# Optimization experiments

Hardware: AMD Instinct MI355X
Metric: run time of the kernel (lower is better)

The kernel has to match this reference:

```python
import jax, jax.numpy as jnp
import numpy as np

T, B, N, L = 1024, 2, 10000, 30   # frames, batch(=2, hardcoded in original), vocab, glosses/sample
S = 2 * L + 1                      # blank-interleaved (CTC-extended) label length


def setup_inputs() -> dict:
    key = jax.random.key(0)
    k1, k2 = jax.random.split(key)
    logits = jax.random.normal(k1, (T, B, N), dtype=jnp.float32)
    label = jax.random.randint(k2, (B * L,), 1, N, dtype=jnp.int32)  # real glosses are >=1 (0 is blank)
    logits_len = jnp.full((B,), T, dtype=jnp.int32)
    label_len = jnp.full((B,), L, dtype=jnp.int32)
    return {"logits": logits, "logits_len": logits_len, "label": label, "label_len": label_len}


def _extend(lab):
    # [l1, l2, ...] -> [0, l1, 0, l2, ..., 0]  (blank-interleaved), shape (S,)
    return jnp.zeros((S,), lab.dtype).at[1::2].set(lab)


def _reach_fwd(ext):
    # map_forward[j, i] > 0  <=>  state j reachable from start at time i (CTC forward lattice).
    pad2 = jnp.full((2,), -1, ext.dtype)
    allow2 = (ext != 0) & (ext != jnp.concatenate([pad2, ext[:-2]]))  # skip-2 allowed
    init = jnp.zeros((S,), bool).at[0].set(True).at[1].set(True)

    def step(c, _):
        s1 = jnp.concatenate([jnp.zeros((1,), bool), c[:-1]])
        s2 = jnp.concatenate([jnp.zeros((2,), bool), c[:-2]]) & allow2
        n = c | s1 | s2
        return n, n

    _, outs = jax.lax.scan(step, init, None, length=T - 1)
    return jnp.concatenate([init[None], outs], axis=0)  # (T, S)


def _reach_bwd(ext):
    # map_backward[j, i] > 0  <=>  end reachable from state j at time i.
    pad2 = jnp.full((2,), -1, ext.dtype)
    allow2 = (ext != 0) & (ext != jnp.concatenate([ext[2:], pad2]))
    init = jnp.zeros((S,), bool).at[S - 1].set(True).at[S - 2].set(True)

    def step(c, _):
        s1 = jnp.concatenate([c[1:], jnp.zeros((1,), bool)])
        s2 = jnp.concatenate([c[2:], jnp.zeros((2,), bool)]) & allow2
        n = c | s1 | s2
        return n, n

    _, outs = jax.lax.scan(step, init, None, length=T - 1)
    return jnp.concatenate([outs[::-1], init[None]], axis=0)  # (T, S), time 0..T-1


def _forward(logits, label):
    labels = label.reshape(B, L)
    ext = jax.vmap(_extend)(labels)            # (B, S)
    rf = jax.vmap(_reach_fwd)(ext)             # (B, T, S)
    rb = jax.vmap(_reach_bwd)(ext)             # (B, T, S)
    sel = (rf & rb).astype(logits.dtype)       # map_final != 0 on the lattice

    def per_sample(logit, e, s):
        # mask[t, v] = any lattice state j with ext[j] == v active at time t
        mask = jnp.zeros((T, N), logit.dtype).at[:, e].max(s) > 0
        # original builds final_label as a detached numpy copy of logit at masked entries
        target = jax.lax.stop_gradient(jnp.where(mask, logit, jnp.zeros((), logit.dtype)))
        return jnp.sum((logit - target) ** 2)  # nn.MSELoss(reduction='sum')

    losses = jax.vmap(per_sample)(jnp.transpose(logits, (1, 0, 2)), ext, sel)
    return jnp.mean(losses)  # (loss1 + loss2) / 2


def reference(logits, logits_len, label, label_len):
    # logits_len / label_len are fixed to full lengths (T, L) so shapes stay static.
    return _forward(logits, label)
```

## Files before the change

### kernel.cpp

```cpp
#include <hip/hip_runtime.h>
#include <stdint.h>

typedef unsigned long long u64;

static constexpr int T = 1024;
static constexpr int B = 2;
static constexpr int N = 10000;
static constexpr int L = 30;
static constexpr int S = 2 * L + 1;

static constexpr int CORR_BLK = 256;
static constexpr int SUM_BLK  = 2048;
static constexpr int NBLK     = CORR_BLK + SUM_BLK;

static constexpr u64 ALL   = (1ULL << S) - 1;
static constexpr u64 EVENM = 0x5555555555555555ULL & ((1ULL << S) - 1);

__device__ __forceinline__ float block_reduce(float s) {
    for (int off = 32; off; off >>= 1) s += __shfl_down(s, off, 64);
    __shared__ float tmp[8];
    int lane = threadIdx.x & 63, w = threadIdx.x >> 6;
    int nw = blockDim.x >> 6;
    if (lane == 0) tmp[w] = s;
    __syncthreads();
    float t = 0.f;
    if (threadIdx.x == 0)
        for (int i = 0; i < nw; ++i) t += tmp[i];
    return t;
}

__global__ void k_fused(const float4* __restrict__ x4, const float* __restrict__ x,
                        const int* __restrict__ label, float* __restrict__ out) {
    float s = 0.f;
    if (blockIdx.x < CORR_BLK) {
        __shared__ int labs[B][L];
        __shared__ u64 dups[B][L];
        __shared__ u64 AfS[B], AbS[B];
        int tid = threadIdx.x;
        if (tid < B) {
            int b = tid;
            int lb[L];
            u64 Af = 0, Ab = 0;
            #pragma unroll
            for (int k = 0; k < L; ++k) { lb[k] = label[b * L + k]; labs[b][k] = lb[k]; }
            #pragma unroll
            for (int k = 0; k < L; ++k) {
                u64 bit = 1ULL << (2 * k + 1);
                if (k == 0     || lb[k] != lb[k - 1]) Af |= bit;
                if (k == L - 1 || lb[k] != lb[k + 1]) Ab |= bit;
                u64 d = 0;
                for (int k2 = 0; k2 < k; ++k2)
                    if (lb[k2] == lb[k]) d |= 1ULL << (2 * k2 + 1);
                dups[b][k] = d;
            }
            AfS[b] = Af; AbS[b] = Ab;
        }
        __syncthreads();
        int pair = blockIdx.x * 8 + (tid >> 5);
        int lane = tid & 31;
        int b = pair >> 10;
        int t = pair & (T - 1);
        u64 m;
        if (t < 64) {
            u64 Af = AfS[b];
            u64 c = 3ULL;
            for (int i = 0; i < t; ++i) c = (c | (c << 1) | ((c << 2) & Af)) & ALL;
            m = c;
        } else if (t >= T - 64) {
            u64 Ab = AbS[b];
            u64 c = (1ULL << (S - 1)) | (1ULL << (S - 2));
            int n = T - 1 - t;
            for (int i = 0; i < n; ++i) c = c | (c >> 1) | ((c >> 2) & Ab);
            m = c;
        } else {
            m = ALL;
        }
        const float* row = x + (size_t)t * (B * N) + (size_t)b * N;
        if (lane < L) {
            u64 bit = 1ULL << (2 * lane + 1);
            if ((m & bit) && !(m & dups[b][lane])) {
                float v = row[labs[b][lane]];
                s -= v * v;
            }
        } else if (lane == L) {
            if (m & EVENM) { float v = row[0]; s -= v * v; }
        }
    } else {
        const int n4 = (T * B * N) / 4;
        int base = (blockIdx.x - CORR_BLK) * blockDim.x + threadIdx.x;
        for (int i = base; i < n4; i += SUM_BLK * 256) {
            float4 v = x4[i];
            s += v.x * v.x + v.y * v.y + v.z * v.z + v.w * v.w;
        }
    }
    float tot = block_reduce(s);
    if (threadIdx.x == 0) atomicAdd(out, 0.5f * tot);
}

extern "C" void kernel_launch(void* const* d_in, const int* in_sizes, int n_in,
                              void* d_out, int out_size, void* d_ws, size_t ws_size,
                              hipStream_t stream) {
    const float* logits = (const float*)d_in[0];
    const int*   label  = (const int*)d_in[2];
    float* out = (float*)d_out;

    hipMemsetAsync(out, 0, sizeof(float), stream);
    k_fused<<<NBLK, 256, 0, stream>>>((const float4*)logits, logits, label, out);
}
```

Baseline: 141.0 us.

## Unroll streaming sum-of-squares 4x, reorder blocks, replace atomics with two-pass reduction

The sum-of-squares blocks now come first in the grid and each thread issues four independent float4 loads per iteration, giving more memory-level parallelism, with fewer sum blocks (1792). The per-block atomicAdd and the memset are replaced by per-block partials in workspace plus a second single-block kernel that sums them. This removes atomic contention and the memset launch but adds a second kernel launch and depends on the workspace being large enough.

New measurement: 120.3 us. 1.17x faster.

```diff
diff --git a/kernel.cpp b/kernel.cpp
--- a/kernel.cpp
+++ b/kernel.cpp
@@ -9,9 +9,9 @@
 static constexpr int L = 30;
 static constexpr int S = 2 * L + 1;
 
+static constexpr int SUM_BLK  = 1792;
 static constexpr int CORR_BLK = 256;
-static constexpr int SUM_BLK  = 2048;
-static constexpr int NBLK     = CORR_BLK + SUM_BLK;
+static constexpr int NBLK     = SUM_BLK + CORR_BLK;
 
 static constexpr u64 ALL   = (1ULL << S) - 1;
 static constexpr u64 EVENM = 0x5555555555555555ULL & ((1ULL << S) - 1);
@@ -29,10 +29,26 @@
     return t;
 }
 
+__device__ __forceinline__ float sq4(float4 v) {
+    return v.x * v.x + v.y * v.y + v.z * v.z + v.w * v.w;
+}
+
 __global__ void k_fused(const float4* __restrict__ x4, const float* __restrict__ x,
-                        const int* __restrict__ label, float* __restrict__ out) {
+                        const int* __restrict__ label, float* __restrict__ partials) {
     float s = 0.f;
-    if (blockIdx.x < CORR_BLK) {
+    if (blockIdx.x < SUM_BLK) {
+        const int n4 = (T * B * N) / 4;
+        const int stride = SUM_BLK * 256;
+        int i0 = blockIdx.x * 256 + threadIdx.x;
+        for (int i = i0; i < n4; i += 4 * stride) {
+            int i1 = i + stride, i2 = i + 2 * stride, i3 = i + 3 * stride;
+            float4 a = x4[i];
+            float4 b = (i1 < n4) ? x4[i1] : make_float4(0.f, 0.f, 0.f, 0.f);
+            float4 c = (i2 < n4) ? x4[i2] : make_float4(0.f, 0.f, 0.f, 0.f);
+            float4 d = (i3 < n4) ? x4[i3] : make_float4(0.f, 0.f, 0.f, 0.f);
+            s += sq4(a) + sq4(b) + sq4(c) + sq4(d);
+        }
+    } else {
         __shared__ int labs[B][L];
         __shared__ u64 dups[B][L];
         __shared__ u64 AfS[B], AbS[B];
@@ -56,7 +72,7 @@
             AfS[b] = Af; AbS[b] = Ab;
         }
         __syncthreads();
-        int pair = blockIdx.x * 8 + (tid >> 5);
+        int pair = (blockIdx.x - SUM_BLK) * 8 + (tid >> 5);
         int lane = tid & 31;
         int b = pair >> 10;
         int t = pair & (T - 1);
@@ -85,16 +101,16 @@
         } else if (lane == L) {
             if (m & EVENM) { float v = row[0]; s -= v * v; }
         }
-    } else {
-        const int n4 = (T * B * N) / 4;
-        int base = (blockIdx.x - CORR_BLK) * blockDim.x + threadIdx.x;
-        for (int i = base; i < n4; i += SUM_BLK * 256) {
-            float4 v = x4[i];
-            s += v.x * v.x + v.y * v.y + v.z * v.z + v.w * v.w;
-        }
     }
     float tot = block_reduce(s);
-    if (threadIdx.x == 0) atomicAdd(out, 0.5f * tot);
+    if (threadIdx.x == 0) partials[blockIdx.x] = tot;
+}
+
+__global__ void k_final(const float* __restrict__ partials, float* __restrict__ out) {
+    float s = 0.f;
+    for (int i = threadIdx.x; i < NBLK; i += 256) s += partials[i];
+    float tot = block_reduce(s);
+    if (threadIdx.x == 0) out[0] = 0.5f * tot;
 }
 
 extern "C" void kernel_launch(void* const* d_in, const int* in_sizes, int n_in,
@@ -102,8 +118,8 @@
                               hipStream_t stream) {
     const float* logits = (const float*)d_in[0];
     const int*   label  = (const int*)d_in[2];
-    float* out = (float*)d_out;
+    float* partials = (float*)d_ws;
 
-    hipMemsetAsync(out, 0, sizeof(float), stream);
-    k_fused<<<NBLK, 256, 0, stream>>>((const float4*)logits, logits, label, out);
+    k_fused<<<NBLK, 256, 0, stream>>>((const float4*)logits, logits, label, partials);
+    k_final<<<1, 256, 0, stream>>>(partials, (float*)d_out);
 }
```
